# Kernel optimization log

Hardware: AMD Instinct MI355X
Metric: run time of the kernel (lower is better)

Reference implementation:

```python
import jax, jax.numpy as jnp
import numpy as np

N = 100000
E = 6400000
IN_CH = 128
HID = 8
HEADS = 2
OUT_CH = 1
NEG_SLOPE = 0.2


def gat_conv(x, src, dst, W, a_src, a_dst, bias, heads, out_ch, concat, n_nodes):
    # x: [N, F_in], W: [F_in, heads*out_ch], a_src/a_dst: [heads, out_ch]
    h = (x @ W).reshape(n_nodes, heads, out_ch)          # [N, H, C]
    alpha_s = jnp.sum(h * a_src[None], axis=-1)          # [N, H]
    alpha_d = jnp.sum(h * a_dst[None], axis=-1)          # [N, H]
    alpha = alpha_s[src] + alpha_d[dst]                  # [E, H]
    alpha = jax.nn.leaky_relu(alpha, NEG_SLOPE)
    # segment softmax over incoming edges of each destination node
    seg_max = jax.ops.segment_max(alpha, dst, num_segments=n_nodes)  # [N, H]
    alpha = jnp.exp(alpha - seg_max[dst])
    denom = jax.ops.segment_sum(alpha, dst, num_segments=n_nodes)    # [N, H]
    alpha = alpha / (denom[dst] + 1e-16)
    msg = h[src] * alpha[..., None]                       # [E, H, C]
    out = jax.ops.segment_sum(msg, dst, num_segments=n_nodes)        # [N, H, C]
    if concat:
        out = out.reshape(n_nodes, heads * out_ch)
    else:
        out = out.mean(axis=1)
    return out + bias


def setup_inputs() -> dict:
    key = jax.random.key(0)
    ks = jax.random.split(key, 12)
    x = jax.random.normal(ks[0], (N, IN_CH), dtype=jnp.float32)
    edge_index = jax.random.randint(ks[1], (2, E), 0, N, dtype=jnp.int64)
    s1 = 1.0 / np.sqrt(IN_CH)
    W1 = jax.random.normal(ks[2], (IN_CH, HEADS * HID), dtype=jnp.float32) * s1
    a_src1 = jax.random.normal(ks[3], (HEADS, HID), dtype=jnp.float32) * (1.0 / np.sqrt(HID))
    a_dst1 = jax.random.normal(ks[4], (HEADS, HID), dtype=jnp.float32) * (1.0 / np.sqrt(HID))
    b1 = jnp.zeros((HEADS * HID,), dtype=jnp.float32)
    s2 = 1.0 / np.sqrt(HEADS * HID)
    W2 = jax.random.normal(ks[5], (HEADS * HID, OUT_CH), dtype=jnp.float32) * s2
    a_src2 = jax.random.normal(ks[6], (1, OUT_CH), dtype=jnp.float32)
    a_dst2 = jax.random.normal(ks[7], (1, OUT_CH), dtype=jnp.float32)
    b2 = jnp.zeros((OUT_CH,), dtype=jnp.float32)
    return {"x": x, "edge_index": edge_index, "W1": W1, "a_src1": a_src1,
            "a_dst1": a_dst1, "b1": b1, "W2": W2, "a_src2": a_src2,
            "a_dst2": a_dst2, "b2": b2}


def reference(x, edge_index, W1, a_src1, a_dst1, b1, W2, a_src2, a_dst2, b2):
    # add self-loops (PyG GATConv default)
    loops = jnp.arange(N, dtype=edge_index.dtype)
    src = jnp.concatenate([edge_index[0], loops])
    dst = jnp.concatenate([edge_index[1], loops])
    h = gat_conv(x, src, dst, W1, a_src1, a_dst1, b1, HEADS, HID, True, N)
    h = jax.nn.relu(h)
    out = gat_conv(h, src, dst, W2, a_src2, a_dst2, b2, 1, OUT_CH, False, N)
    return out
```

## Files before the change

kernel.cpp:

```cpp
#include <hip/hip_runtime.h>
#include <hip/hip_fp16.h>
#include <cstdint>
#include <cstddef>

#define N_NODES 100000
#define E_EDGES 6400000
#define E_TOT   (E_EDGES + N_NODES)
#define IN_CH   128
#define NHID    16
#define BSHIFT  9
#define BSZ     512
#define NBUCK   196
#define CHUNK   6144
#define BCAP    72
#define NCHUNK  ((E_TOT + CHUNK - 1) / CHUNK)

__global__ void k_detect(const int* __restrict__ edge, int* __restrict__ flag) {
    if (blockIdx.x == 0 && threadIdx.x == 0) {
        int odd_or = 0;
        for (int i = 0; i < 64; i++) odd_or |= edge[2 * i + 1];
        flag[0] = (odd_or == 0) ? 1 : 0;
    }
}

__device__ __forceinline__ int load_src(const int* e, size_t i, int m64) {
    return m64 ? e[2 * i] : e[i];
}
__device__ __forceinline__ int load_dst(const int* e, size_t i, int m64) {
    return m64 ? e[2 * ((size_t)E_EDGES + i)] : e[(size_t)E_EDGES + i];
}

__global__ __launch_bounds__(256) void k_gemm1(
        const float* __restrict__ x, const float* __restrict__ W1,
        const float* __restrict__ a_src1, const float* __restrict__ a_dst1,
        __half* __restrict__ h16, float* __restrict__ asrc,
        float* __restrict__ adst) {
    __shared__ __align__(16) float sW[IN_CH * NHID];
    __shared__ __align__(16) float sx[16][132];
    __shared__ float sh[16][17];
    int t = threadIdx.x;
    int r = t >> 4, c = t & 15;
    int row = blockIdx.x * 16 + r;

    const float4* W4 = (const float4*)W1;
    ((float4*)sW)[t] = W4[t];
    ((float4*)sW)[t + 256] = W4[t + 256];

    if (row < N_NODES) {
        const float4* xr = (const float4*)(x + (size_t)row * IN_CH);
        float4 v0 = xr[c];
        float4 v1 = xr[c + 16];
        *(float4*)&sx[r][4 * c] = v0;
        *(float4*)&sx[r][64 + 4 * c] = v1;
    }
    __syncthreads();

    float acc = 0.f;
    if (row < N_NODES) {
        #pragma unroll 16
        for (int k = 0; k < IN_CH; k++) acc = fmaf(sx[r][k], sW[k * NHID + c], acc);
        h16[(size_t)row * NHID + c] = __float2half(acc);
    }
    sh[r][c] = acc;
    __syncthreads();

    if (row < N_NODES && c < 4) {
        int h = c & 1;
        const float* av = (c >= 2) ? a_dst1 : a_src1;
        float s = 0.f;
        #pragma unroll
        for (int q = 0; q < 8; q++) s = fmaf(sh[r][h * 8 + q], av[h * 8 + q], s);
        if (c < 2) asrc[2 * (size_t)row + c] = s;
        else       adst[2 * (size_t)row + (c - 2)] = s;
    }
}

__global__ __launch_bounds__(256) void k_ccount(const int* __restrict__ edge,
                                                const int* __restrict__ flag,
                                                int* __restrict__ ccnt) {
    __shared__ int sc[NBUCK];
    int m64 = flag[0];
    int t = threadIdx.x;
    for (int i = t; i < NBUCK; i += 256) sc[i] = 0;
    __syncthreads();
    size_t c0 = (size_t)blockIdx.x * CHUNK;
    size_t cend = c0 + CHUNK; if (cend > E_TOT) cend = E_TOT;
    size_t ee = (cend < (size_t)E_EDGES) ? cend : (size_t)E_EDGES;

    if (m64) {
        const int4* dp = (const int4*)(edge + 2 * (size_t)E_EDGES);
        for (size_t i = c0 + 2 * t; i < ee; i += 512) {
            int4 v = dp[i >> 1];
            atomicAdd(&sc[v.x >> BSHIFT], 1);
            if (i + 1 < ee) atomicAdd(&sc[v.z >> BSHIFT], 1);
        }
    } else {
        const int4* dp = (const int4*)(edge + (size_t)E_EDGES);
        for (size_t i = c0 + 4 * t; i < ee; i += 1024) {
            int4 v = dp[i >> 2];
            atomicAdd(&sc[v.x >> BSHIFT], 1);
            if (i + 1 < ee) atomicAdd(&sc[v.y >> BSHIFT], 1);
            if (i + 2 < ee) atomicAdd(&sc[v.z >> BSHIFT], 1);
            if (i + 3 < ee) atomicAdd(&sc[v.w >> BSHIFT], 1);
        }
    }
    size_t sl0 = (c0 > (size_t)E_EDGES) ? c0 : (size_t)E_EDGES;
    for (size_t i = sl0 + t; i < cend; i += 256) {
        int d = (int)(i - E_EDGES);
        atomicAdd(&sc[d >> BSHIFT], 1);
    }
    __syncthreads();
    for (int i = t; i < NBUCK; i += 256)
        ccnt[(size_t)blockIdx.x * NBUCK + i] = sc[i];
}

__global__ __launch_bounds__(256) void k_cscan(int* __restrict__ ccnt,
                                               int* __restrict__ bcnt) {
    __shared__ int sd[256];
    __shared__ int carry;
    int b = blockIdx.x, t = threadIdx.x;
    if (t == 0) carry = 0;
    __syncthreads();
    for (int base = 0; base < NCHUNK; base += 256) {
        int c = base + t;
        int v = (c < NCHUNK) ? ccnt[(size_t)c * NBUCK + b] : 0;
        sd[t] = v;
        __syncthreads();
        for (int ofs = 1; ofs < 256; ofs <<= 1) {
            int a = sd[t];
            int bb = (t >= ofs) ? sd[t - ofs] : 0;
            __syncthreads();
            sd[t] = a + bb;
            __syncthreads();
        }
        if (c < NCHUNK) ccnt[(size_t)c * NBUCK + b] = sd[t] - v + carry;
        __syncthreads();
        if (t == 255) carry += sd[255];
        __syncthreads();
    }
    if (t == 0) bcnt[b] = carry;
}

__global__ void k_bscan(const int* __restrict__ bcnt, int* __restrict__ bbase) {
    __shared__ int sd[256];
    int t = threadIdx.x;
    int v = (t < NBUCK) ? bcnt[t] : 0;
    sd[t] = v;
    __syncthreads();
    for (int ofs = 1; ofs < 256; ofs <<= 1) {
        int a = sd[t];
        int b = (t >= ofs) ? sd[t - ofs] : 0;
        __syncthreads();
        sd[t] = a + b;
        __syncthreads();
    }
    if (t < NBUCK) bbase[t] = sd[t] - v;
    if (t == NBUCK) bbase[NBUCK] = sd[NBUCK - 1];
}

__global__ __launch_bounds__(256) void k_bin(const int* __restrict__ edge,
                                             const int* __restrict__ flag,
                                             const int* __restrict__ ccnt,
                                             const int* __restrict__ bbase,
                                             unsigned* __restrict__ staged) {
    __shared__ unsigned lbin[NBUCK][BCAP];
    __shared__ int lcnt[NBUCK];
    __shared__ int lbase[NBUCK];
    int m64 = flag[0];
    int t = threadIdx.x;
    int g = t >> 4, lane = t & 15;

    size_t c0 = (size_t)blockIdx.x * CHUNK;
    if (c0 >= E_TOT) return;
    size_t cend = c0 + CHUNK; if (cend > E_TOT) cend = E_TOT;
    size_t ee = (cend < (size_t)E_EDGES) ? cend : (size_t)E_EDGES;

    for (int i = t; i < NBUCK; i += 256) {
        lcnt[i] = 0;
        lbase[i] = bbase[i] + ccnt[(size_t)blockIdx.x * NBUCK + i];
    }
    __syncthreads();

    auto put = [&](int s, int d) {
        int b = d >> BSHIFT;
        unsigned v = (unsigned)s | ((unsigned)(d & (BSZ - 1)) << 17);
        int idx = atomicAdd(&lcnt[b], 1);
        if (idx < BCAP) lbin[b][idx] = v;
        else            staged[lbase[b] + idx] = v;
    };

    if (m64) {
        const int4* sp = (const int4*)edge;
        const int4* dp = (const int4*)(edge + 2 * (size_t)E_EDGES);
        for (size_t i = c0 + 2 * t; i < ee; i += 512) {
            int4 sv = sp[i >> 1];
            int4 dv = dp[i >> 1];
            put(sv.x, dv.x);
            if (i + 1 < ee) put(sv.z, dv.z);
        }
    } else {
        const int4* sp = (const int4*)edge;
        const int4* dp = (const int4*)(edge + (size_t)E_EDGES);
        for (size_t i = c0 + 4 * t; i < ee; i += 1024) {
            int4 sv = sp[i >> 2];
            int4 dv = dp[i >> 2];
            put(sv.x, dv.x);
            if (i + 1 < ee) put(sv.y, dv.y);
            if (i + 2 < ee) put(sv.z, dv.z);
            if (i + 3 < ee) put(sv.w, dv.w);
        }
    }
    size_t sl0 = (c0 > (size_t)E_EDGES) ? c0 : (size_t)E_EDGES;
    for (size_t i = sl0 + t; i < cend; i += 256) {
        int d = (int)(i - E_EDGES);
        put(d, d);
    }
    __syncthreads();
    for (int b = g; b < NBUCK; b += 16) {
        int n = min(lcnt[b], BCAP);
        if (!n) continue;
        int pos = lbase[b];
        for (int i = lane; i < n; i += 16) staged[pos + i] = lbin[b][i];
    }
}

__global__ __launch_bounds__(1024) void k_sort(const unsigned* __restrict__ staged,
                                               const int* __restrict__ bbase,
                                               int* __restrict__ csr,
                                               int* __restrict__ offs) {
    __shared__ int hist[BSZ];
    __shared__ int histlo[BSZ];
    __shared__ int lcur[BSZ];
    int bkt = blockIdx.x >> 1, p = blockIdx.x & 1;
    int t = threadIdx.x;
    int beg = bbase[bkt], end = bbase[bkt + 1];
    int mid = beg + ((end - beg + 1) >> 1);
    int dbase = bkt << BSHIFT;

    if (t < BSZ) { hist[t] = 0; histlo[t] = 0; }
    __syncthreads();
    for (int e = beg + t; e < end; e += 1024) {
        int dl = staged[e] >> 17;
        atomicAdd(&hist[dl], 1);
        if (e < mid) atomicAdd(&histlo[dl], 1);
    }
    __syncthreads();

    int myv = (t < BSZ) ? hist[t] : 0;
    __syncthreads();
    for (int ofs = 1; ofs < BSZ; ofs <<= 1) {
        int a = 0, b = 0;
        if (t < BSZ) { a = hist[t]; b = (t >= ofs) ? hist[t - ofs] : 0; }
        __syncthreads();
        if (t < BSZ) hist[t] = a + b;
        __syncthreads();
    }
    if (t < BSZ) {
        int excl = hist[t] - myv;
        lcur[t] = excl + (p ? histlo[t] : 0);
        if (p == 0) {
            int dd = dbase + t;
            if (dd < N_NODES) offs[dd] = beg + excl;
        }
    }
    if (bkt == NBUCK - 1 && p == 0 && t == 0) offs[N_NODES] = E_TOT;
    __syncthreads();

    int lo = p ? mid : beg;
    int hi = p ? end : mid;
    for (int e = lo + t; e < hi; e += 1024) {
        unsigned v = staged[e];
        int pos = atomicAdd(&lcur[v >> 17], 1);
        csr[beg + pos] = (int)(v & 0x1FFFFu);
    }
}

__global__ __launch_bounds__(256) void k_edge1(
        const int* __restrict__ offs, const int* __restrict__ csr,
        const __half* __restrict__ h16, const float* __restrict__ asrc,
        const float* __restrict__ adst,
        const float* __restrict__ b1, const float* __restrict__ W2,
        float* __restrict__ h2out) {
    __shared__ float sacc[256][17];
    int t = threadIdx.x;
    int lane = t & 15;
    int g = t >> 4;
    int d = blockIdx.x * 16 + g;
    if (d >= N_NODES) return;

    float2 adp = ((const float2*)adst)[d];
    int beg = offs[d], end = offs[d + 1];

    float acc[16];
    #pragma unroll
    for (int c = 0; c < 16; c++) acc[c] = 0.f;
    float den0 = 0.f, den1 = 0.f;

    auto loadslot = [&](int ee, float2& asp, float4& r0, float4& r1) {
        if (ee < end) {
            int s = csr[ee];
            asp = ((const float2*)asrc)[s];
            const float4* hp = (const float4*)(h16 + (size_t)s * NHID);
            r0 = hp[0]; r1 = hp[1];
        }
    };
    auto consume = [&](const float2& asp, const float4& r0, const float4& r1) {
        float a0 = asp.x + adp.x; a0 = (a0 > 0.f) ? a0 : 0.2f * a0;
        float a1 = asp.y + adp.y; a1 = (a1 > 0.f) ? a1 : 0.2f * a1;
        float p0 = __expf(a0), p1 = __expf(a1);
        den0 += p0; den1 += p1;
        const __half2* h0 = (const __half2*)&r0;
        const __half2* h1 = (const __half2*)&r1;
        #pragma unroll
        for (int q = 0; q < 4; q++) {
            float2 f0 = __half22float2(h0[q]);
            float2 f1 = __half22float2(h1[q]);
            acc[2 * q]         = fmaf(p0, f0.x, acc[2 * q]);
            acc[2 * q + 1]     = fmaf(p0, f0.y, acc[2 * q + 1]);
            acc[8 + 2 * q]     = fmaf(p1, f1.x, acc[8 + 2 * q]);
            acc[8 + 2 * q + 1] = fmaf(p1, f1.y, acc[8 + 2 * q + 1]);
        }
    };

    float2 aspA{}, aspB{}, aspC{}, aspD{};
    float4 z4 = make_float4(0.f, 0.f, 0.f, 0.f);
    float4 r0A = z4, r1A = z4, r0B = z4, r1B = z4;
    float4 r0C = z4, r1C = z4, r0D = z4, r1D = z4;

    int e = beg + lane;
    loadslot(e,      aspA, r0A, r1A);
    loadslot(e + 16, aspB, r0B, r1B);
    loadslot(e + 32, aspC, r0C, r1C);
    loadslot(e + 48, aspD, r0D, r1D);
    while (true) {
        if (e >= end) break;
        consume(aspA, r0A, r1A); loadslot(e + 64, aspA, r0A, r1A); e += 16;
        if (e >= end) break;
        consume(aspB, r0B, r1B); loadslot(e + 64, aspB, r0B, r1B); e += 16;
        if (e >= end) break;
        consume(aspC, r0C, r1C); loadslot(e + 64, aspC, r0C, r1C); e += 16;
        if (e >= end) break;
        consume(aspD, r0D, r1D); loadslot(e + 64, aspD, r0D, r1D); e += 16;
    }
    #pragma unroll
    for (int m = 1; m < 16; m <<= 1) {
        den0 += __shfl_xor(den0, m, 64);
        den1 += __shfl_xor(den1, m, 64);
    }
    #pragma unroll
    for (int c = 0; c < 16; c++) sacc[t][c] = acc[c];
    float sum = 0.f;
    int rowb = g * 16;
    #pragma unroll
    for (int l = 0; l < 16; l++) sum += sacc[rowb + l][lane];

    float den = (lane < 8) ? den0 : den1;
    float o = sum / (den + 1e-16f) + b1[lane];
    o = (o > 0.f) ? o : 0.f;
    float v = o * W2[lane];
    v += __shfl_xor(v, 1, 64);
    v += __shfl_xor(v, 2, 64);
    v += __shfl_xor(v, 4, 64);
    v += __shfl_xor(v, 8, 64);
    if (lane == 0) h2out[d] = v;
}

__global__ __launch_bounds__(256) void k_edge2(
        const int* __restrict__ offs, const int* __restrict__ csr,
        const float* __restrict__ h2,
        const float* __restrict__ a_src2, const float* __restrict__ a_dst2,
        const float* __restrict__ b2, float* __restrict__ out) {
    int t = threadIdx.x;
    int g = t >> 4, lane = t & 15;
    int d = blockIdx.x * 16 + g;
    if (d >= N_NODES) return;

    float as2 = a_src2[0], ad2 = a_dst2[0];
    float adv = h2[d] * ad2;
    int beg = offs[d], end = offs[d + 1];

    float den = 0.f, acc = 0.f;
    auto ls = [&](int ee, float& hs) { if (ee < end) hs = h2[csr[ee]]; };
    auto cs = [&](float hs) {
        float a = fmaf(hs, as2, adv);
        a = (a > 0.f) ? a : 0.2f * a;
        float p = __expf(a);
        den += p;
        acc = fmaf(p, hs, acc);
    };
    float hA = 0.f, hB = 0.f, hC = 0.f, hD = 0.f;
    int e = beg + lane;
    ls(e, hA); ls(e + 16, hB); ls(e + 32, hC); ls(e + 48, hD);
    while (true) {
        if (e >= end) break;
        cs(hA); ls(e + 64, hA); e += 16;
        if (e >= end) break;
        cs(hB); ls(e + 64, hB); e += 16;
        if (e >= end) break;
        cs(hC); ls(e + 64, hC); e += 16;
        if (e >= end) break;
        cs(hD); ls(e + 64, hD); e += 16;
    }
    #pragma unroll
    for (int m = 1; m < 16; m <<= 1) {
        den += __shfl_xor(den, m, 64);
        acc += __shfl_xor(acc, m, 64);
    }
    if (lane == 0) out[d] = acc / (den + 1e-16f) + b2[0];
}

extern "C" void kernel_launch(void* const* d_in, const int* in_sizes, int n_in,
                              void* d_out, int out_size, void* d_ws, size_t ws_size,
                              hipStream_t stream) {
    const float* x      = (const float*)d_in[0];
    const int*   edge   = (const int*)  d_in[1];
    const float* W1     = (const float*)d_in[2];
    const float* a_src1 = (const float*)d_in[3];
    const float* a_dst1 = (const float*)d_in[4];
    const float* b1     = (const float*)d_in[5];
    const float* W2     = (const float*)d_in[6];
    const float* a_src2 = (const float*)d_in[7];
    const float* a_dst2 = (const float*)d_in[8];
    const float* b2     = (const float*)d_in[9];

    constexpr size_t A = 256;
    auto al = [](size_t b) { return (b + A - 1) / A * A; };
    char* ws = (char*)d_ws;
    size_t off = 0;
    int*      flag   = (int*)(ws + off);      off += al(256);
    int*      ccnt   = (int*)(ws + off);      off += al((size_t)NCHUNK * NBUCK * 4);
    int*      bcnt   = (int*)(ws + off);      off += al(NBUCK * 4);
    int*      bbase  = (int*)(ws + off);      off += al((NBUCK + 1) * 4);
    unsigned* staged = (unsigned*)(ws + off); off += al((size_t)E_TOT * 4);
    int*      csr    = (int*)(ws + off);      off += al((size_t)E_TOT * 4);
    int*      offs   = (int*)(ws + off);      off += al((size_t)(N_NODES + 1) * 4);
    __half*   h16    = (__half*)(ws + off);   off += al((size_t)N_NODES * NHID * 2);
    float*    asrc   = (float*)(ws + off);    off += al((size_t)N_NODES * 2 * 4);
    float*    adst   = (float*)(ws + off);    off += al((size_t)N_NODES * 2 * 4);
    float*    h2     = (float*)(ws + off);    off += al((size_t)N_NODES * 4);
    (void)ws_size; (void)in_sizes; (void)n_in; (void)out_size;

    k_detect<<<1, 64, 0, stream>>>(edge, flag);
    k_gemm1 <<<(N_NODES + 15) / 16, 256, 0, stream>>>(x, W1, a_src1, a_dst1, h16, asrc, adst);
    k_ccount<<<NCHUNK, 256, 0, stream>>>(edge, flag, ccnt);
    k_cscan <<<NBUCK, 256, 0, stream>>>(ccnt, bcnt);
    k_bscan <<<1, 256, 0, stream>>>(bcnt, bbase);
    k_bin   <<<NCHUNK, 256, 0, stream>>>(edge, flag, ccnt, bbase, staged);
    k_sort  <<<NBUCK * 2, 1024, 0, stream>>>(staged, bbase, csr, offs);
    k_edge1 <<<(N_NODES + 15) / 16, 256, 0, stream>>>(offs, csr, h16, asrc, adst, b1, W2, h2);
    k_edge2 <<<(N_NODES + 15) / 16, 256, 0, stream>>>(offs, csr, h2, a_src2, a_dst2, b2,
                                                      (float*)d_out);
}
```

Baseline: 238.6 us.

## Pack per-node features and source logits into one record, deepen gather prefetch

Interleaves each node's fp16 hidden features and source attention logits into a single 64-byte record, so an edge gather reads one cache line instead of two separate arrays. Both edge-aggregation kernels raise their software prefetch depth from four to six slots per lane to keep more gathers in flight. BCAP is also reduced. The extra prefetch slots raise register pressure, and the 64-byte padded record uses more memory than the 40 bytes of data it holds.

New measurement: 219.3 us. 1.09x faster.

```diff
diff --git a/kernel.cpp b/kernel.cpp
--- a/kernel.cpp
+++ b/kernel.cpp
@@ -8,11 +8,12 @@
 #define E_TOT   (E_EDGES + N_NODES)
 #define IN_CH   128
 #define NHID    16
+#define RECB    64
 #define BSHIFT  9
 #define BSZ     512
 #define NBUCK   196
 #define CHUNK   6144
-#define BCAP    72
+#define BCAP    48
 #define NCHUNK  ((E_TOT + CHUNK - 1) / CHUNK)
 
 __global__ void k_detect(const int* __restrict__ edge, int* __restrict__ flag) {
@@ -23,18 +24,10 @@
     }
 }
 
-__device__ __forceinline__ int load_src(const int* e, size_t i, int m64) {
-    return m64 ? e[2 * i] : e[i];
-}
-__device__ __forceinline__ int load_dst(const int* e, size_t i, int m64) {
-    return m64 ? e[2 * ((size_t)E_EDGES + i)] : e[(size_t)E_EDGES + i];
-}
-
 __global__ __launch_bounds__(256) void k_gemm1(
         const float* __restrict__ x, const float* __restrict__ W1,
         const float* __restrict__ a_src1, const float* __restrict__ a_dst1,
-        __half* __restrict__ h16, float* __restrict__ asrc,
-        float* __restrict__ adst) {
+        char* __restrict__ rec, float* __restrict__ adst) {
     __shared__ __align__(16) float sW[IN_CH * NHID];
     __shared__ __align__(16) float sx[16][132];
     __shared__ float sh[16][17];
@@ -59,7 +52,7 @@
     if (row < N_NODES) {
         #pragma unroll 16
         for (int k = 0; k < IN_CH; k++) acc = fmaf(sx[r][k], sW[k * NHID + c], acc);
-        h16[(size_t)row * NHID + c] = __float2half(acc);
+        ((__half*)(rec + (size_t)row * RECB))[c] = __float2half(acc);
     }
     sh[r][c] = acc;
     __syncthreads();
@@ -70,7 +63,7 @@
         float s = 0.f;
         #pragma unroll
         for (int q = 0; q < 8; q++) s = fmaf(sh[r][h * 8 + q], av[h * 8 + q], s);
-        if (c < 2) asrc[2 * (size_t)row + c] = s;
+        if (c < 2) ((float*)(rec + (size_t)row * RECB + 32))[c] = s;
         else       adst[2 * (size_t)row + (c - 2)] = s;
     }
 }
@@ -277,8 +270,7 @@
 
 __global__ __launch_bounds__(256) void k_edge1(
         const int* __restrict__ offs, const int* __restrict__ csr,
-        const __half* __restrict__ h16, const float* __restrict__ asrc,
-        const float* __restrict__ adst,
+        const char* __restrict__ rec, const float* __restrict__ adst,
         const float* __restrict__ b1, const float* __restrict__ W2,
         float* __restrict__ h2out) {
     __shared__ float sacc[256][17];
@@ -299,9 +291,10 @@
     auto loadslot = [&](int ee, float2& asp, float4& r0, float4& r1) {
         if (ee < end) {
             int s = csr[ee];
-            asp = ((const float2*)asrc)[s];
-            const float4* hp = (const float4*)(h16 + (size_t)s * NHID);
-            r0 = hp[0]; r1 = hp[1];
+            const char* rp = rec + (size_t)s * RECB;
+            r0 = ((const float4*)rp)[0];
+            r1 = ((const float4*)rp)[1];
+            asp = *(const float2*)(rp + 32);
         }
     };
     auto consume = [&](const float2& asp, const float4& r0, const float4& r1) {
@@ -322,25 +315,31 @@
         }
     };
 
-    float2 aspA{}, aspB{}, aspC{}, aspD{};
+    float2 aspA{}, aspB{}, aspC{}, aspD{}, aspE{}, aspF{};
     float4 z4 = make_float4(0.f, 0.f, 0.f, 0.f);
-    float4 r0A = z4, r1A = z4, r0B = z4, r1B = z4;
-    float4 r0C = z4, r1C = z4, r0D = z4, r1D = z4;
+    float4 r0A = z4, r1A = z4, r0B = z4, r1B = z4, r0C = z4, r1C = z4;
+    float4 r0D = z4, r1D = z4, r0E = z4, r1E = z4, r0F = z4, r1F = z4;
 
     int e = beg + lane;
     loadslot(e,      aspA, r0A, r1A);
     loadslot(e + 16, aspB, r0B, r1B);
     loadslot(e + 32, aspC, r0C, r1C);
     loadslot(e + 48, aspD, r0D, r1D);
+    loadslot(e + 64, aspE, r0E, r1E);
+    loadslot(e + 80, aspF, r0F, r1F);
     while (true) {
         if (e >= end) break;
-        consume(aspA, r0A, r1A); loadslot(e + 64, aspA, r0A, r1A); e += 16;
-        if (e >= end) break;
-        consume(aspB, r0B, r1B); loadslot(e + 64, aspB, r0B, r1B); e += 16;
-        if (e >= end) break;
-        consume(aspC, r0C, r1C); loadslot(e + 64, aspC, r0C, r1C); e += 16;
-        if (e >= end) break;
-        consume(aspD, r0D, r1D); loadslot(e + 64, aspD, r0D, r1D); e += 16;
+        consume(aspA, r0A, r1A); loadslot(e + 96, aspA, r0A, r1A); e += 16;
+        if (e >= end) break;
+        consume(aspB, r0B, r1B); loadslot(e + 96, aspB, r0B, r1B); e += 16;
+        if (e >= end) break;
+        consume(aspC, r0C, r1C); loadslot(e + 96, aspC, r0C, r1C); e += 16;
+        if (e >= end) break;
+        consume(aspD, r0D, r1D); loadslot(e + 96, aspD, r0D, r1D); e += 16;
+        if (e >= end) break;
+        consume(aspE, r0E, r1E); loadslot(e + 96, aspE, r0E, r1E); e += 16;
+        if (e >= end) break;
+        consume(aspF, r0F, r1F); loadslot(e + 96, aspF, r0F, r1F); e += 16;
     }
     #pragma unroll
     for (int m = 1; m < 16; m <<= 1) {
@@ -388,18 +387,23 @@
         den += p;
         acc = fmaf(p, hs, acc);
     };
-    float hA = 0.f, hB = 0.f, hC = 0.f, hD = 0.f;
+    float hA = 0.f, hB = 0.f, hC = 0.f, hD = 0.f, hE = 0.f, hF = 0.f;
     int e = beg + lane;
-    ls(e, hA); ls(e + 16, hB); ls(e + 32, hC); ls(e + 48, hD);
+    ls(e, hA); ls(e + 16, hB); ls(e + 32, hC);
+    ls(e + 48, hD); ls(e + 64, hE); ls(e + 80, hF);
     while (true) {
         if (e >= end) break;
-        cs(hA); ls(e + 64, hA); e += 16;
-        if (e >= end) break;
-        cs(hB); ls(e + 64, hB); e += 16;
-        if (e >= end) break;
-        cs(hC); ls(e + 64, hC); e += 16;
-        if (e >= end) break;
-        cs(hD); ls(e + 64, hD); e += 16;
+        cs(hA); ls(e + 96, hA); e += 16;
+        if (e >= end) break;
+        cs(hB); ls(e + 96, hB); e += 16;
+        if (e >= end) break;
+        cs(hC); ls(e + 96, hC); e += 16;
+        if (e >= end) break;
+        cs(hD); ls(e + 96, hD); e += 16;
+        if (e >= end) break;
+        cs(hE); ls(e + 96, hE); e += 16;
+        if (e >= end) break;
+        cs(hF); ls(e + 96, hF); e += 16;
     }
     #pragma unroll
     for (int m = 1; m < 16; m <<= 1) {
@@ -434,20 +438,19 @@
     unsigned* staged = (unsigned*)(ws + off); off += al((size_t)E_TOT * 4);
     int*      csr    = (int*)(ws + off);      off += al((size_t)E_TOT * 4);
     int*      offs   = (int*)(ws + off);      off += al((size_t)(N_NODES + 1) * 4);
-    __half*   h16    = (__half*)(ws + off);   off += al((size_t)N_NODES * NHID * 2);
-    float*    asrc   = (float*)(ws + off);    off += al((size_t)N_NODES * 2 * 4);
+    char*     rec    = (char*)(ws + off);     off += al((size_t)N_NODES * RECB);
     float*    adst   = (float*)(ws + off);    off += al((size_t)N_NODES * 2 * 4);
     float*    h2     = (float*)(ws + off);    off += al((size_t)N_NODES * 4);
     (void)ws_size; (void)in_sizes; (void)n_in; (void)out_size;
 
     k_detect<<<1, 64, 0, stream>>>(edge, flag);
-    k_gemm1 <<<(N_NODES + 15) / 16, 256, 0, stream>>>(x, W1, a_src1, a_dst1, h16, asrc, adst);
+    k_gemm1 <<<(N_NODES + 15) / 16, 256, 0, stream>>>(x, W1, a_src1, a_dst1, rec, adst);
     k_ccount<<<NCHUNK, 256, 0, stream>>>(edge, flag, ccnt);
     k_cscan <<<NBUCK, 256, 0, stream>>>(ccnt, bcnt);
     k_bscan <<<1, 256, 0, stream>>>(bcnt, bbase);
     k_bin   <<<NCHUNK, 256, 0, stream>>>(edge, flag, ccnt, bbase, staged);
     k_sort  <<<NBUCK * 2, 1024, 0, stream>>>(staged, bbase, csr, offs);
-    k_edge1 <<<(N_NODES + 15) / 16, 256, 0, stream>>>(offs, csr, h16, asrc, adst, b1, W2, h2);
+    k_edge1 <<<(N_NODES + 15) / 16, 256, 0, stream>>>(offs, csr, rec, adst, b1, W2, h2);
     k_edge2 <<<(N_NODES + 15) / 16, 256, 0, stream>>>(offs, csr, h2, a_src2, a_dst2, b2,
                                                       (float*)d_out);
 }
```
